# Optimization experiments

Hardware: AMD Instinct MI355X
Metric: run time of the kernel (lower is better)

The kernel has to match this reference:

```python
import jax, jax.numpy as jnp
import numpy as np

B, T, H = 128, 256, 512


def setup_inputs() -> dict:
    key = jax.random.key(0)
    ks = jax.random.split(key, 9)
    s = 0.05  # small init scale to keep tanh/softmax well-conditioned
    return {
        "enc_output": jax.random.normal(ks[0], (B, T, H), jnp.float32),
        "h0": jax.random.normal(ks[1], (B, H), jnp.float32) * s,
        "c0": jax.random.normal(ks[2], (B, H), jnp.float32) * s,
        "W1": jax.random.normal(ks[3], (H, H), jnp.float32) * s,
        "W2": jax.random.normal(ks[4], (H, H), jnp.float32) * s,
        "V": jax.random.normal(ks[5], (H,), jnp.float32) * s,
        "Wk": jax.random.normal(ks[6], (T, 4 * H), jnp.float32) * s,  # LSTM input kernel (input = last_pointer, dim T)
        "Wr": jax.random.normal(ks[7], (H, 4 * H), jnp.float32) * s,  # LSTM recurrent kernel
        "b": jnp.zeros((4 * H,), jnp.float32),
    }


def reference(enc_output, h0, c0, W1, W2, V, Wk, Wr, b):
    Bq, Tq, Hq = enc_output.shape
    # Precompute W1 @ encoder outputs (constant across decode steps; same math)
    w1_e = jnp.einsum("bth,hd->btd", enc_output, W1)  # [B,T,H]

    def step(carry, _):
        h, c, lp = carry  # h,c: [B,H]; lp (last pointer probs): [B,T]
        z = lp @ Wk + h @ Wr + b  # [B,4H], keras gate order i,f,g,o
        i, f, g, o = jnp.split(z, 4, axis=-1)
        c_new = jax.nn.sigmoid(f) * c + jax.nn.sigmoid(i) * jnp.tanh(g)
        h_new = jax.nn.sigmoid(o) * jnp.tanh(c_new)
        # Bahdanau additive attention -> pointer distribution over T
        w2_d = h_new @ W2  # [B,H]
        score = jnp.einsum("bth,h->bt", jnp.tanh(w1_e + w2_d[:, None, :]), V)  # [B,T]
        probs = jax.nn.softmax(score, axis=1)
        return (h_new, c_new, probs), probs

    lp0 = jnp.ones((Bq, Tq), enc_output.dtype)
    _, outs = jax.lax.scan(step, (h0, c0, lp0), None, length=Tq)  # [T,B,T]
    return jnp.transpose(outs, (1, 0, 2))  # [B, T(steps), T(pointers)]
```

## Files before the change

### kernel.cpp

```cpp
#include <hip/hip_runtime.h>
#include <hip/hip_bf16.h>
#include <cstddef>

#define B_ 128
#define T_ 256
#define H_ 512
#define H4_ 2048

__device__ __forceinline__ float rcp_f(float x) { return __builtin_amdgcn_rcpf(x); }
__device__ __forceinline__ float sigf(float x) { return rcp_f(1.0f + __expf(-x)); }
__device__ __forceinline__ float tanh_f(float x) {
  float p = __expf(x + x);
  return fmaf(-2.0f, rcp_f(1.0f + p), 1.0f);
}
__device__ __forceinline__ float4 ld4(const float* p) { return *reinterpret_cast<const float4*>(p); }
__device__ __forceinline__ void st4(float* p, float4 v) { *reinterpret_cast<float4*>(p) = v; }
__device__ __forceinline__ void fma4(float4& a, float s, float4 w) {
  a.x = fmaf(s, w.x, a.x); a.y = fmaf(s, w.y, a.y);
  a.z = fmaf(s, w.z, a.z); a.w = fmaf(s, w.w, a.w);
}

__device__ __forceinline__ float ald1(const float* p) {
  return __hip_atomic_load(p, __ATOMIC_RELAXED, __HIP_MEMORY_SCOPE_AGENT);
}
__device__ __forceinline__ void ast1(float* p, float v) {
  __hip_atomic_store(p, v, __ATOMIC_RELAXED, __HIP_MEMORY_SCOPE_AGENT);
}
__device__ __forceinline__ float2 ald2(const float* p) {
  unsigned long long v = __hip_atomic_load((const unsigned long long*)p,
                                           __ATOMIC_RELAXED, __HIP_MEMORY_SCOPE_AGENT);
  union { unsigned long long u; float2 f; } c; c.u = v; return c.f;
}

#define W1E_OFF   0ull
#define WPACK_OFF 16777216ull
#define HP_OFF    18350080ull
#define HROW_OFF  18481152ull
#define EP_OFF    18546688ull
#define W2D_OFF   18579456ull
#define D2_OFF    18644992ull
#define CNT_OFF   18645504ull

__global__ __launch_bounds__(256) void w1e_kernel(const float* __restrict__ A,
                                                  const float* __restrict__ Bw,
                                                  float* __restrict__ C) {
  __shared__ float As[32][68];
  __shared__ float Bs[32][68];
  const int i0 = blockIdx.x * 64;
  const int j0 = blockIdx.y * 64;
  const int tx = threadIdx.x & 15, ty = threadIdx.x >> 4;
  float4 acc0 = make_float4(0,0,0,0), acc1 = acc0, acc2 = acc0, acc3 = acc0;
  for (int k0 = 0; k0 < H_; k0 += 32) {
#pragma unroll
    for (int q = 0; q < 2; q++) {
      int idx = q * 256 + threadIdx.x;
      int ai = idx >> 3, ak = (idx & 7) << 2;
      float4 av = ld4(A + (size_t)(i0 + ai) * H_ + k0 + ak);
      As[ak][ai] = av.x; As[ak + 1][ai] = av.y; As[ak + 2][ai] = av.z; As[ak + 3][ai] = av.w;
      int bk = idx >> 4, bj = (idx & 15) << 2;
      st4(&Bs[bk][bj], ld4(Bw + (size_t)(k0 + bk) * H_ + j0 + bj));
    }
    __syncthreads();
#pragma unroll
    for (int kk = 0; kk < 32; kk++) {
      float4 a = ld4(&As[kk][ty << 2]);
      float4 bv = ld4(&Bs[kk][tx << 2]);
      fma4(acc0, a.x, bv); fma4(acc1, a.y, bv); fma4(acc2, a.z, bv); fma4(acc3, a.w, bv);
    }
    __syncthreads();
  }
  size_t base = (size_t)(i0 + (ty << 2)) * H_ + j0 + (tx << 2);
  st4(&C[base], acc0); st4(&C[base + H_], acc1);
  st4(&C[base + 2 * H_], acc2); st4(&C[base + 3 * H_], acc3);
}

__global__ __launch_bounds__(256) void pack_kernel(const float* __restrict__ Wk,
                                                   const float* __restrict__ Wr,
                                                   float* __restrict__ Wpack,
                                                   unsigned* __restrict__ cnt) {
  const int g = blockIdx.x, tid = threadIdx.x;
#pragma unroll
  for (int it = 0; it < 24; ++it) {
    int idx = it * 256 + tid;
    int k = idx >> 3, c = idx & 7;
    int col = (c >> 1) * 512 + 2 * g + (c & 1);
    float v = (k < 256) ? Wk[(size_t)k * H4_ + col] : Wr[(size_t)(k - 256) * H4_ + col];
    Wpack[((size_t)g * 768 + k) * 8 + c] = v;
  }
  if (g == 0) {
#pragma unroll
    for (int i = 0; i < 4; ++i) cnt[i * 256 + tid] = 0u;
  }
}

__device__ __forceinline__ void gridbar(unsigned* cnt, unsigned& phase, int tid, int wg) {
  asm volatile("s_waitcnt vmcnt(0)" ::: "memory");
  __syncthreads();
  if (tid == 0) {
    unsigned r1 = __hip_atomic_fetch_add(&cnt[(wg & 31) * 16], 1u,
                                         __ATOMIC_RELAXED, __HIP_MEMORY_SCOPE_AGENT);
    if (r1 == phase * 8u + 7u) {
      unsigned r2 = __hip_atomic_fetch_add(&cnt[512], 1u,
                                           __ATOMIC_RELAXED, __HIP_MEMORY_SCOPE_AGENT);
      if (r2 == phase * 32u + 31u) {
#pragma unroll
        for (int i = 0; i < 8; ++i)
          __hip_atomic_store(&cnt[768 + i * 16], phase + 1u,
                             __ATOMIC_RELAXED, __HIP_MEMORY_SCOPE_AGENT);
      }
    }
    const unsigned* rel = &cnt[768 + (wg >> 5) * 16];
    while (__hip_atomic_load(rel, __ATOMIC_RELAXED, __HIP_MEMORY_SCOPE_AGENT) <= phase)
      __builtin_amdgcn_s_sleep(4);
  }
  __syncthreads();
  ++phase;
}

__global__ __launch_bounds__(1024, 4) void decoder_persistent(
    const float* __restrict__ w1e, const float* __restrict__ Wpack,
    const float* __restrict__ W2, const float* __restrict__ Vv,
    const float* __restrict__ bias, const float* __restrict__ h0,
    const float* __restrict__ c0,
    float* __restrict__ htr,
    float* __restrict__ hrow,
    float* __restrict__ etr,
    float* __restrict__ w2dA,
    float* __restrict__ d2,
    unsigned* __restrict__ cnt,
    float* __restrict__ out) {
  __shared__ float smem[21504];
  float* zred     = smem;
  float* zfin     = smem + 12288;
  float* c_lds    = smem + 13312;
  float* bias_lds = smem + 13568;
  float* dred     = smem + 13576;

  const int g = blockIdx.x;
  const int tid = threadIdx.x;
  const int bl = tid & 127;
  const int ksu = __builtin_amdgcn_readfirstlane(tid >> 7);
  const int wv = tid >> 6, ln = tid & 63;
  const int sb = g >> 1;
  const int t0 = (g & 1) << 7;
  unsigned phase = 0;
  float epv[8];

  if (tid < 256) {
    int b = tid >> 1, jj = tid & 1;
    c_lds[b * 2 + jj] = c0[(size_t)b * H_ + 2 * g + jj];
    ast1(htr + 65536 + ((size_t)g * 128 + b) * 2 + jj, h0[(size_t)b * H_ + 2 * g + jj]);
    if (g == 0) ast1(d2 + 256 + tid, 0.5f);
  }
  if (tid < 8) bias_lds[tid] = bias[(tid >> 1) * 512 + 2 * g + (tid & 1)];
  if (g < 128) ast1(etr + g * 256 + tid, 1.0f);
  gridbar(cnt, phase, tid, g);

  const float4 v0 = ld4(Vv + (ln << 3));
  const float4 v1 = ld4(Vv + (ln << 3) + 4);

  for (int s = 0; s < 256; ++s) {
    const float* hin = htr + ((s + 1) & 1) * 65536;
    float* hout = htr + (s & 1) * 65536;
    const float* dPrev = d2 + ((s + 1) & 1) * 256;
    float* dCur = d2 + (s & 1) * 256;

    {
      float2 dd = ald2(dPrev + bl * 2);
      float rd = rcp_f(dd.x + dd.y);
      float4 accA = make_float4(0,0,0,0), accB = accA;
#pragma unroll 4
      for (int j = 0; j < 8; ++j) {
        int kb = ksu * 4 + j * 32;
        float2 i0 = ald2(etr + (kb >> 1) * 256 + bl * 2);
        float2 i1 = ald2(etr + (kb >> 1) * 256 + 256 + bl * 2);
        const float* wp = Wpack + (((size_t)g * 768 + kb) << 3);
        float4 wa0 = ld4(wp),      wb0 = ld4(wp + 4);
        float4 wa1 = ld4(wp + 8),  wb1 = ld4(wp + 12);
        float4 wa2 = ld4(wp + 16), wb2 = ld4(wp + 20);
        float4 wa3 = ld4(wp + 24), wb3 = ld4(wp + 28);
        fma4(accA, i0.x, wa0); fma4(accB, i0.x, wb0);
        fma4(accA, i0.y, wa1); fma4(accB, i0.y, wb1);
        fma4(accA, i1.x, wa2); fma4(accB, i1.x, wb2);
        fma4(accA, i1.y, wa3); fma4(accB, i1.y, wb3);
      }
      accA.x *= rd; accA.y *= rd; accA.z *= rd; accA.w *= rd;
      accB.x *= rd; accB.y *= rd; accB.z *= rd; accB.w *= rd;
#pragma unroll 4
      for (int j = 0; j < 16; ++j) {
        int kb = ksu * 4 + j * 32;
        float2 i0 = ald2(hin + (kb >> 1) * 256 + bl * 2);
        float2 i1 = ald2(hin + (kb >> 1) * 256 + 256 + bl * 2);
        const float* wp = Wpack + (((size_t)g * 768 + 256 + kb) << 3);
        float4 wa0 = ld4(wp),      wb0 = ld4(wp + 4);
        float4 wa1 = ld4(wp + 8),  wb1 = ld4(wp + 12);
        float4 wa2 = ld4(wp + 16), wb2 = ld4(wp + 20);
        float4 wa3 = ld4(wp + 24), wb3 = ld4(wp + 28);
        fma4(accA, i0.x, wa0); fma4(accB, i0.x, wb0);
        fma4(accA, i0.y, wa1); fma4(accB, i0.y, wb1);
        fma4(accA, i1.x, wa2); fma4(accB, i1.x, wb2);
        fma4(accA, i1.y, wa3); fma4(accB, i1.y, wb3);
      }
      float* zr = &zred[(ksu * 128 + bl) * 12];
      st4(zr, accA); st4(zr + 4, accB);
    }
    __syncthreads();
    {
      int b = tid >> 3, cc = tid & 7;
      float zsum = bias_lds[cc];
#pragma unroll
      for (int k2 = 0; k2 < 8; ++k2) zsum += zred[(k2 * 128 + b) * 12 + cc];
      zfin[b * 8 + cc] = zsum;
    }
    __syncthreads();
    if (tid < 256) {
      int b = tid >> 1, jj = tid & 1;
      float zi = zfin[b * 8 + 0 + jj], zf = zfin[b * 8 + 2 + jj];
      float zg = zfin[b * 8 + 4 + jj], zo = zfin[b * 8 + 6 + jj];
      float cv = c_lds[b * 2 + jj];
      float cn = sigf(zf) * cv + sigf(zi) * tanh_f(zg);
      float hn = sigf(zo) * tanh_f(cn);
      c_lds[b * 2 + jj] = cn;
      ast1(hout + ((size_t)g * 128 + b) * 2 + jj, hn);
      ast1(hrow + (size_t)b * 512 + 2 * g + jj, hn);
    }
    gridbar(cnt, phase, tid, g);

    {
      const int ci = t0 + (t0 ? 256 - 128 : 0);
      const int colb = ((g & 1) << 8) + (ln << 2);
      (void)ci;
      float4 acc = make_float4(0,0,0,0);
      const float* hb = hrow + (size_t)sb * 512 + (wv << 5);
#pragma unroll 8
      for (int kk = 0; kk < 32; ++kk) {
        float hk = ald1(hb + kk);
        float4 wr2 = ld4(W2 + (size_t)((wv << 5) + kk) * 512 + colb);
        fma4(acc, hk, wr2);
      }
      st4(&zred[(wv << 8) + (ln << 2)], acc);
    }
    __syncthreads();
    if (tid < 256) {
      float sum = 0.0f;
#pragma unroll
      for (int w = 0; w < 16; ++w) sum += zred[(w << 8) + tid];
      ast1(w2dA + (size_t)sb * 512 + ((g & 1) << 8) + tid, sum);
    }
    gridbar(cnt, phase, tid, g);

    {
      const float* wrow = w2dA + (size_t)sb * 512 + (ln << 3);
      float2 a0 = ald2(wrow), a1 = ald2(wrow + 2), a2 = ald2(wrow + 4), a3 = ald2(wrow + 6);
      float4 u0 = make_float4(a0.x, a0.y, a1.x, a1.y);
      float4 u1 = make_float4(a2.x, a2.y, a3.x, a3.y);
      float2 ddp = ald2(dPrev + sb * 2);
      float rdp = rcp_f(ddp.x + ddp.y);
      float dacc = 0.0f;
#pragma unroll
      for (int r = 0; r < 8; ++r) {
        int t = t0 + (wv << 3) + r;
        const float* row = w1e + (((size_t)sb * 256 + t) << 9) + (ln << 3);
        float4 x0 = ld4(row), x1 = ld4(row + 4);
        float a;
        a = tanh_f(x0.x + u0.x) * v0.x;
        a = fmaf(tanh_f(x0.y + u0.y), v0.y, a);
        a = fmaf(tanh_f(x0.z + u0.z), v0.z, a);
        a = fmaf(tanh_f(x0.w + u0.w), v0.w, a);
        a = fmaf(tanh_f(x1.x + u1.x), v1.x, a);
        a = fmaf(tanh_f(x1.y + u1.y), v1.y, a);
        a = fmaf(tanh_f(x1.z + u1.z), v1.z, a);
        a = fmaf(tanh_f(x1.w + u1.w), v1.w, a);
#pragma unroll
        for (int m = 32; m > 0; m >>= 1) a += __shfl_xor(a, m, 64);
        if (ln == 0) {
          if (s > 0) out[(size_t)sb * 65536 + (size_t)(s - 1) * 256 + t] = epv[r] * rdp;
          float ev = __expf(a);
          epv[r] = ev;
          ast1(etr + (((t >> 1) << 7) + sb) * 2 + (t & 1), ev);
          dacc += ev;
        }
      }
      if (ln == 0) dred[wv] = dacc;
    }
    __syncthreads();
    if (tid == 0) {
      float sd = 0.0f;
#pragma unroll
      for (int k = 0; k < 16; ++k) sd += dred[k];
      ast1(dCur + sb * 2 + (g & 1), sd);
    }
    gridbar(cnt, phase, tid, g);
  }

  {
    float2 ddf = ald2(d2 + 256 + sb * 2);
    float rdf = rcp_f(ddf.x + ddf.y);
    if (ln == 0) {
#pragma unroll
      for (int r = 0; r < 8; ++r) {
        int t = t0 + (wv << 3) + r;
        out[(size_t)sb * 65536 + 255ull * 256 + t] = epv[r] * rdf;
      }
    }
  }
}

extern "C" void kernel_launch(void* const* d_in, const int* in_sizes, int n_in,
                              void* d_out, int out_size, void* d_ws, size_t ws_size,
                              hipStream_t stream) {
  const float* enc  = (const float*)d_in[0];
  const float* h0   = (const float*)d_in[1];
  const float* c0   = (const float*)d_in[2];
  const float* W1   = (const float*)d_in[3];
  const float* W2   = (const float*)d_in[4];
  const float* V    = (const float*)d_in[5];
  const float* Wk   = (const float*)d_in[6];
  const float* Wr   = (const float*)d_in[7];
  const float* bias = (const float*)d_in[8];
  float* out = (float*)d_out;
  float* ws = (float*)d_ws;

  float* w1e    = ws + W1E_OFF;
  float* Wpack  = ws + WPACK_OFF;
  float* htr    = ws + HP_OFF;
  float* hrow   = ws + HROW_OFF;
  float* etr    = ws + EP_OFF;
  float* w2dA   = ws + W2D_OFF;
  float* d2     = ws + D2_OFF;
  unsigned* cnt = (unsigned*)(ws + CNT_OFF);

  pack_kernel<<<256, 256, 0, stream>>>(Wk, Wr, Wpack, cnt);
  w1e_kernel<<<dim3(512, 8), 256, 0, stream>>>(enc, W1, w1e);
  decoder_persistent<<<256, 1024, 0, stream>>>(w1e, Wpack, W2, V, bias, h0, c0,
                                               htr, hrow, etr, w2dA, d2, cnt, out);
}
```

Measured before the change: 9.360 ms.

## Store W1·enc and W2 in fp16 and batch atomic loads ahead of FMAs

Stores the precomputed W1·enc tensor and W2 as half precision in the workspace, halving the bytes streamed by the attention and W2 stages on every decode step. The LSTM gate loops and the W2 loop now issue all their atomic input loads up front before the FMAs, so load latency can overlap. The grid-barrier spin sleep is also shortened. This trades numeric precision in the attention scores for bandwidth and uses more registers.

```diff
diff --git a/kernel.cpp b/kernel.cpp
--- a/kernel.cpp
+++ b/kernel.cpp
@@ -32,18 +32,28 @@
   union { unsigned long long u; float2 f; } c; c.u = v; return c.f;
 }
 
-#define W1E_OFF   0ull
-#define WPACK_OFF 16777216ull
-#define HP_OFF    18350080ull
-#define HROW_OFF  18481152ull
-#define EP_OFF    18546688ull
-#define W2D_OFF   18579456ull
-#define D2_OFF    18644992ull
-#define CNT_OFF   18645504ull
+union H4 { ushort4 u; _Float16 h[4]; };
+union H8 { int4 v; _Float16 h[8]; };
+__device__ __forceinline__ void sth4(_Float16* p, float4 v) {
+  H4 c;
+  c.h[0] = (_Float16)v.x; c.h[1] = (_Float16)v.y;
+  c.h[2] = (_Float16)v.z; c.h[3] = (_Float16)v.w;
+  *reinterpret_cast<ushort4*>(p) = c.u;
+}
+
+#define W1EH_OFF  0ull
+#define WPACK_OFF 8388608ull
+#define W2H_OFF   9961472ull
+#define HP_OFF    10092544ull
+#define HROW_OFF  10223616ull
+#define EP_OFF    10289152ull
+#define W2D_OFF   10321920ull
+#define D2_OFF    10387456ull
+#define CNT_OFF   10387968ull
 
 __global__ __launch_bounds__(256) void w1e_kernel(const float* __restrict__ A,
                                                   const float* __restrict__ Bw,
-                                                  float* __restrict__ C) {
+                                                  _Float16* __restrict__ C) {
   __shared__ float As[32][68];
   __shared__ float Bs[32][68];
   const int i0 = blockIdx.x * 64;
@@ -70,13 +80,15 @@
     __syncthreads();
   }
   size_t base = (size_t)(i0 + (ty << 2)) * H_ + j0 + (tx << 2);
-  st4(&C[base], acc0); st4(&C[base + H_], acc1);
-  st4(&C[base + 2 * H_], acc2); st4(&C[base + 3 * H_], acc3);
+  sth4(&C[base], acc0); sth4(&C[base + H_], acc1);
+  sth4(&C[base + 2 * H_], acc2); sth4(&C[base + 3 * H_], acc3);
 }
 
 __global__ __launch_bounds__(256) void pack_kernel(const float* __restrict__ Wk,
                                                    const float* __restrict__ Wr,
+                                                   const float* __restrict__ W2,
                                                    float* __restrict__ Wpack,
+                                                   _Float16* __restrict__ W2h,
                                                    unsigned* __restrict__ cnt) {
   const int g = blockIdx.x, tid = threadIdx.x;
 #pragma unroll
@@ -86,6 +98,11 @@
     int col = (c >> 1) * 512 + 2 * g + (c & 1);
     float v = (k < 256) ? Wk[(size_t)k * H4_ + col] : Wr[(size_t)(k - 256) * H4_ + col];
     Wpack[((size_t)g * 768 + k) * 8 + c] = v;
+  }
+#pragma unroll
+  for (int it = 0; it < 4; ++it) {
+    int idx = it * 65536 + g * 256 + tid;
+    W2h[idx] = (_Float16)W2[idx];
   }
   if (g == 0) {
 #pragma unroll
@@ -111,15 +128,15 @@
     }
     const unsigned* rel = &cnt[768 + (wg >> 5) * 16];
     while (__hip_atomic_load(rel, __ATOMIC_RELAXED, __HIP_MEMORY_SCOPE_AGENT) <= phase)
-      __builtin_amdgcn_s_sleep(4);
+      __builtin_amdgcn_s_sleep(2);
   }
   __syncthreads();
   ++phase;
 }
 
 __global__ __launch_bounds__(1024, 4) void decoder_persistent(
-    const float* __restrict__ w1e, const float* __restrict__ Wpack,
-    const float* __restrict__ W2, const float* __restrict__ Vv,
+    const _Float16* __restrict__ w1eh, const float* __restrict__ Wpack,
+    const _Float16* __restrict__ W2h, const float* __restrict__ Vv,
     const float* __restrict__ bias, const float* __restrict__ h0,
     const float* __restrict__ c0,
     float* __restrict__ htr,
@@ -169,37 +186,50 @@
       float2 dd = ald2(dPrev + bl * 2);
       float rd = rcp_f(dd.x + dd.y);
       float4 accA = make_float4(0,0,0,0), accB = accA;
-#pragma unroll 4
+      float2 e0[8], e1[8];
+#pragma unroll
+      for (int j = 0; j < 8; ++j) {
+        int k2 = ksu * 2 + j * 16;
+        e0[j] = ald2(etr + k2 * 256 + bl * 2);
+        e1[j] = ald2(etr + k2 * 256 + 256 + bl * 2);
+      }
+#pragma unroll
       for (int j = 0; j < 8; ++j) {
         int kb = ksu * 4 + j * 32;
-        float2 i0 = ald2(etr + (kb >> 1) * 256 + bl * 2);
-        float2 i1 = ald2(etr + (kb >> 1) * 256 + 256 + bl * 2);
         const float* wp = Wpack + (((size_t)g * 768 + kb) << 3);
         float4 wa0 = ld4(wp),      wb0 = ld4(wp + 4);
         float4 wa1 = ld4(wp + 8),  wb1 = ld4(wp + 12);
         float4 wa2 = ld4(wp + 16), wb2 = ld4(wp + 20);
         float4 wa3 = ld4(wp + 24), wb3 = ld4(wp + 28);
-        fma4(accA, i0.x, wa0); fma4(accB, i0.x, wb0);
-        fma4(accA, i0.y, wa1); fma4(accB, i0.y, wb1);
-        fma4(accA, i1.x, wa2); fma4(accB, i1.x, wb2);
-        fma4(accA, i1.y, wa3); fma4(accB, i1.y, wb3);
+        fma4(accA, e0[j].x, wa0); fma4(accB, e0[j].x, wb0);
+        fma4(accA, e0[j].y, wa1); fma4(accB, e0[j].y, wb1);
+        fma4(accA, e1[j].x, wa2); fma4(accB, e1[j].x, wb2);
+        fma4(accA, e1[j].y, wa3); fma4(accB, e1[j].y, wb3);
       }
       accA.x *= rd; accA.y *= rd; accA.z *= rd; accA.w *= rd;
       accB.x *= rd; accB.y *= rd; accB.z *= rd; accB.w *= rd;
-#pragma unroll 4
-      for (int j = 0; j < 16; ++j) {
-        int kb = ksu * 4 + j * 32;
-        float2 i0 = ald2(hin + (kb >> 1) * 256 + bl * 2);
-        float2 i1 = ald2(hin + (kb >> 1) * 256 + 256 + bl * 2);
-        const float* wp = Wpack + (((size_t)g * 768 + 256 + kb) << 3);
-        float4 wa0 = ld4(wp),      wb0 = ld4(wp + 4);
-        float4 wa1 = ld4(wp + 8),  wb1 = ld4(wp + 12);
-        float4 wa2 = ld4(wp + 16), wb2 = ld4(wp + 20);
-        float4 wa3 = ld4(wp + 24), wb3 = ld4(wp + 28);
-        fma4(accA, i0.x, wa0); fma4(accB, i0.x, wb0);
-        fma4(accA, i0.y, wa1); fma4(accB, i0.y, wb1);
-        fma4(accA, i1.x, wa2); fma4(accB, i1.x, wb2);
-        fma4(accA, i1.y, wa3); fma4(accB, i1.y, wb3);
+#pragma unroll
+      for (int half = 0; half < 2; ++half) {
+        float2 p0[8], p1[8];
+#pragma unroll
+        for (int j = 0; j < 8; ++j) {
+          int k2 = ksu * 2 + (half * 8 + j) * 16;
+          p0[j] = ald2(hin + k2 * 256 + bl * 2);
+          p1[j] = ald2(hin + k2 * 256 + 256 + bl * 2);
+        }
+#pragma unroll
+        for (int j = 0; j < 8; ++j) {
+          int kb = ksu * 4 + (half * 8 + j) * 32;
+          const float* wp = Wpack + (((size_t)g * 768 + 256 + kb) << 3);
+          float4 wa0 = ld4(wp),      wb0 = ld4(wp + 4);
+          float4 wa1 = ld4(wp + 8),  wb1 = ld4(wp + 12);
+          float4 wa2 = ld4(wp + 16), wb2 = ld4(wp + 20);
+          float4 wa3 = ld4(wp + 24), wb3 = ld4(wp + 28);
+          fma4(accA, p0[j].x, wa0); fma4(accB, p0[j].x, wb0);
+          fma4(accA, p0[j].y, wa1); fma4(accB, p0[j].y, wb1);
+          fma4(accA, p1[j].x, wa2); fma4(accB, p1[j].x, wb2);
+          fma4(accA, p1[j].y, wa3); fma4(accB, p1[j].y, wb3);
+        }
       }
       float* zr = &zred[(ksu * 128 + bl) * 12];
       st4(zr, accA); st4(zr + 4, accB);
@@ -227,16 +257,17 @@
     gridbar(cnt, phase, tid, g);
 
     {
-      const int ci = t0 + (t0 ? 256 - 128 : 0);
       const int colb = ((g & 1) << 8) + (ln << 2);
-      (void)ci;
+      const float* hb = hrow + (size_t)sb * 512 + (wv << 5);
+      float hreg[32];
+#pragma unroll
+      for (int kk = 0; kk < 32; ++kk) hreg[kk] = ald1(hb + kk);
       float4 acc = make_float4(0,0,0,0);
-      const float* hb = hrow + (size_t)sb * 512 + (wv << 5);
 #pragma unroll 8
       for (int kk = 0; kk < 32; ++kk) {
-        float hk = ald1(hb + kk);
-        float4 wr2 = ld4(W2 + (size_t)((wv << 5) + kk) * 512 + colb);
-        fma4(acc, hk, wr2);
+        H4 w; w.u = *reinterpret_cast<const ushort4*>(W2h + (size_t)((wv << 5) + kk) * 512 + colb);
+        float4 wf = make_float4((float)w.h[0], (float)w.h[1], (float)w.h[2], (float)w.h[3]);
+        fma4(acc, hreg[kk], wf);
       }
       st4(&zred[(wv << 8) + (ln << 2)], acc);
     }
@@ -256,32 +287,40 @@
       float4 u1 = make_float4(a2.x, a2.y, a3.x, a3.y);
       float2 ddp = ald2(dPrev + sb * 2);
       float rdp = rcp_f(ddp.x + ddp.y);
-      float dacc = 0.0f;
+      const _Float16* rowb = w1eh + (((size_t)sb * 256 + t0 + (wv << 3)) << 9) + (ln << 3);
+      H8 raws[8];
+#pragma unroll
+      for (int r = 0; r < 8; ++r)
+        raws[r].v = *reinterpret_cast<const int4*>(rowb + (size_t)r * 512);
+      float sc[8];
 #pragma unroll
       for (int r = 0; r < 8; ++r) {
-        int t = t0 + (wv << 3) + r;
-        const float* row = w1e + (((size_t)sb * 256 + t) << 9) + (ln << 3);
-        float4 x0 = ld4(row), x1 = ld4(row + 4);
         float a;
-        a = tanh_f(x0.x + u0.x) * v0.x;
-        a = fmaf(tanh_f(x0.y + u0.y), v0.y, a);
-        a = fmaf(tanh_f(x0.z + u0.z), v0.z, a);
-        a = fmaf(tanh_f(x0.w + u0.w), v0.w, a);
-        a = fmaf(tanh_f(x1.x + u1.x), v1.x, a);
-        a = fmaf(tanh_f(x1.y + u1.y), v1.y, a);
-        a = fmaf(tanh_f(x1.z + u1.z), v1.z, a);
-        a = fmaf(tanh_f(x1.w + u1.w), v1.w, a);
+        a = tanh_f((float)raws[r].h[0] + u0.x) * v0.x;
+        a = fmaf(tanh_f((float)raws[r].h[1] + u0.y), v0.y, a);
+        a = fmaf(tanh_f((float)raws[r].h[2] + u0.z), v0.z, a);
+        a = fmaf(tanh_f((float)raws[r].h[3] + u0.w), v0.w, a);
+        a = fmaf(tanh_f((float)raws[r].h[4] + u1.x), v1.x, a);
+        a = fmaf(tanh_f((float)raws[r].h[5] + u1.y), v1.y, a);
+        a = fmaf(tanh_f((float)raws[r].h[6] + u1.z), v1.z, a);
+        a = fmaf(tanh_f((float)raws[r].h[7] + u1.w), v1.w, a);
 #pragma unroll
         for (int m = 32; m > 0; m >>= 1) a += __shfl_xor(a, m, 64);
-        if (ln == 0) {
+        sc[r] = a;
+      }
+      if (ln == 0) {
+        float dacc = 0.0f;
+#pragma unroll
+        for (int r = 0; r < 8; ++r) {
+          int t = t0 + (wv << 3) + r;
           if (s > 0) out[(size_t)sb * 65536 + (size_t)(s - 1) * 256 + t] = epv[r] * rdp;
-          float ev = __expf(a);
+          float ev = __expf(sc[r]);
           epv[r] = ev;
           ast1(etr + (((t >> 1) << 7) + sb) * 2 + (t & 1), ev);
           dacc += ev;
         }
-      }
-      if (ln == 0) dred[wv] = dacc;
+        dred[wv] = dacc;
+      }
     }
     __syncthreads();
     if (tid == 0) {
@@ -321,17 +360,18 @@
   float* out = (float*)d_out;
   float* ws = (float*)d_ws;
 
-  float* w1e    = ws + W1E_OFF;
-  float* Wpack  = ws + WPACK_OFF;
-  float* htr    = ws + HP_OFF;
-  float* hrow   = ws + HROW_OFF;
-  float* etr    = ws + EP_OFF;
-  float* w2dA   = ws + W2D_OFF;
-  float* d2     = ws + D2_OFF;
-  unsigned* cnt = (unsigned*)(ws + CNT_OFF);
-
-  pack_kernel<<<256, 256, 0, stream>>>(Wk, Wr, Wpack, cnt);
-  w1e_kernel<<<dim3(512, 8), 256, 0, stream>>>(enc, W1, w1e);
-  decoder_persistent<<<256, 1024, 0, stream>>>(w1e, Wpack, W2, V, bias, h0, c0,
+  _Float16* w1eh = (_Float16*)(ws + W1EH_OFF);
+  float* Wpack   = ws + WPACK_OFF;
+  _Float16* W2h  = (_Float16*)(ws + W2H_OFF);
+  float* htr     = ws + HP_OFF;
+  float* hrow    = ws + HROW_OFF;
+  float* etr     = ws + EP_OFF;
+  float* w2dA    = ws + W2D_OFF;
+  float* d2      = ws + D2_OFF;
+  unsigned* cnt  = (unsigned*)(ws + CNT_OFF);
+
+  pack_kernel<<<256, 256, 0, stream>>>(Wk, Wr, W2, Wpack, W2h, cnt);
+  w1e_kernel<<<dim3(512, 8), 256, 0, stream>>>(enc, W1, w1eh);
+  decoder_persistent<<<256, 1024, 0, stream>>>(w1eh, Wpack, W2h, V, bias, h0, c0,
                                                htr, hrow, etr, w2dA, d2, cnt, out);
 }
```

Measured after the change: 10.08 ms. +7.7%, slower.
